# Optimization experiments

Hardware: AMD Instinct MI355X
Metric: run time of the kernel (lower is better)

Reference implementation:

```python
import jax, jax.numpy as jnp
import numpy as np


def _temperature():
    # Reproduce the per-class temperature from RIDE.__init__
    cls_num_list = np.array([705, 717, 281, 4772, 1982, 1290, 2524], dtype=np.float64)
    p = cls_num_list / cls_num_list.sum()
    C = len(cls_num_list)
    w = C * p * 0.015 + 1 - 0.015
    w = w / w.max()
    return jnp.asarray(1.5 * w, dtype=jnp.float32)[None, :]  # (1, C)


def setup_inputs() -> dict:
    key = jax.random.key(0)
    k1, k2, k3, k4, k5 = jax.random.split(key, 5)
    N, C = 2097152, 7
    return {
        "outputs1": jax.random.normal(k1, (N, C), dtype=jnp.float32),
        "outputs2": jax.random.normal(k2, (N, C), dtype=jnp.float32),
        "outputs3": jax.random.normal(k3, (N, C), dtype=jnp.float32),
        "outputs4": jax.random.normal(k4, (N, C), dtype=jnp.float32),
        "targets": jax.random.randint(k5, (N,), 0, C, dtype=jnp.int64),
    }


def reference(outputs1, outputs2, outputs3, outputs4, targets):
    # targets is unused by the original loss math (only logits enter the KL terms).
    T = _temperature()                       # (1, C), broadcasts over batch
    mT2 = jnp.mean(T * T)                    # scalar: mean over classes of T^2

    z0 = outputs1 / T                        # (N, C)
    q = jax.nn.softmax(z0, axis=-1)          # teacher probs
    logq = jax.nn.log_softmax(z0, axis=-1)

    def kl_mean(out_j):
        # KLDivLoss(reduction='mean') over a single-sample (1, C) slice == mean over C
        lp = jax.nn.log_softmax(out_j / T, axis=-1)
        return jnp.mean(q * (logq - lp), axis=-1)  # (N,)

    cost = kl_mean(outputs2) + kl_mean(outputs3) + kl_mean(outputs4)  # (N,)
    # KD_loss (scalar) * T * T then .mean(1) == KD_loss * mean(T^2); d = cost/3
    loss = cost * mT2 / 3.0
    return jnp.mean(loss)
```

## Files before the change

kernel.cpp:

```cpp
#include <hip/hip_runtime.h>


struct RideConsts {
    float invT[7];
    float scale;
};


#define STUDENT_ROW(R, c0, c1, c2, c3, c4, c5, c6) do {                      \
    const float z0 = (c0) * iT0, z1 = (c1) * iT1, z2 = (c2) * iT2,           \
                z3 = (c3) * iT3, z4 = (c4) * iT4, z5 = (c5) * iT5,           \
                z6 = (c6) * iT6;                                             \
    const float m = fmaxf(fmaxf(fmaxf(z0, z1), fmaxf(z2, z3)),              \
                          fmaxf(fmaxf(z4, z5), z6));                         \
    const float S = __expf(z0 - m) + __expf(z1 - m) + __expf(z2 - m) +       \
                    __expf(z3 - m) + __expf(z4 - m) + __expf(z5 - m) +       \
                    __expf(z6 - m);                                          \
    zs##R##0 += z0; zs##R##1 += z1; zs##R##2 += z2; zs##R##3 += z3;          \
    zs##R##4 += z4; zs##R##5 += z5; zs##R##6 += z6;                          \
    mls##R += m + __logf(S);                                                 \
} while (0)

#define TEACHER_ROW(R, c0, c1, c2, c3, c4, c5, c6) do {                      \
    const float z0 = (c0) * iT0, z1 = (c1) * iT1, z2 = (c2) * iT2,           \
                z3 = (c3) * iT3, z4 = (c4) * iT4, z5 = (c5) * iT5,           \
                z6 = (c6) * iT6;                                             \
    const float m = fmaxf(fmaxf(fmaxf(z0, z1), fmaxf(z2, z3)),              \
                          fmaxf(fmaxf(z4, z5), z6));                         \
    const float e0 = __expf(z0 - m), e1 = __expf(z1 - m),                    \
                e2 = __expf(z2 - m), e3 = __expf(z3 - m),                    \
                e4 = __expf(z4 - m), e5 = __expf(z5 - m),                    \
                e6 = __expf(z6 - m);                                         \
    const float S = e0 + e1 + e2 + e3 + e4 + e5 + e6;                        \
    const float invS = 1.0f / S, mlogS = m + __logf(S);                      \
    const float q0 = e0 * invS, q1 = e1 * invS, q2 = e2 * invS,              \
                q3 = e3 * invS, q4 = e4 * invS, q5 = e5 * invS,              \
                q6 = e6 * invS;                                              \
    const float qz = q0 * z0 + q1 * z1 + q2 * z2 + q3 * z3 + q4 * z4 +       \
                     q5 * z5 + q6 * z6;                                      \
    const float dot = q0 * zs##R##0 + q1 * zs##R##1 + q2 * zs##R##2 +        \
                      q3 * zs##R##3 + q4 * zs##R##4 + q5 * zs##R##5 +        \
                      q6 * zs##R##6;                                         \
    cost += 3.0f * (qz - mlogS) - dot + mls##R;                              \
} while (0)

#define DO_ARRAY(ROWM, ptr) do {                                             \
    const float4* gp = (const float4*)(ptr) + base;                          \
    const float4 g0 = gp[0], g1 = gp[1], g2 = gp[2], g3 = gp[3],             \
                 g4 = gp[4], g5 = gp[5], g6 = gp[6];                         \
    ROWM(0, g0.x, g0.y, g0.z, g0.w, g1.x, g1.y, g1.z);                       \
    ROWM(1, g1.w, g2.x, g2.y, g2.z, g2.w, g3.x, g3.y);                       \
    ROWM(2, g3.z, g3.w, g4.x, g4.y, g4.z, g4.w, g5.x);                       \
    ROWM(3, g5.y, g5.z, g5.w, g6.x, g6.y, g6.z, g6.w);                       \
} while (0)

__global__ __launch_bounds__(256, 5) void ride_main(
    const float* __restrict__ x1, const float* __restrict__ x2,
    const float* __restrict__ x3, const float* __restrict__ x4,
    float* __restrict__ partials, RideConsts cst)
{
    const int t = threadIdx.x;
    const int w = t >> 6;
    const int L = t & 63;
    const int waveId = blockIdx.x * 4 + w;

    const size_t base = (size_t)waveId * 448 + (size_t)L * 7;

    const float iT0 = cst.invT[0], iT1 = cst.invT[1], iT2 = cst.invT[2],
                iT3 = cst.invT[3], iT4 = cst.invT[4], iT5 = cst.invT[5],
                iT6 = cst.invT[6];

    float zs00 = 0, zs01 = 0, zs02 = 0, zs03 = 0, zs04 = 0, zs05 = 0, zs06 = 0;
    float zs10 = 0, zs11 = 0, zs12 = 0, zs13 = 0, zs14 = 0, zs15 = 0, zs16 = 0;
    float zs20 = 0, zs21 = 0, zs22 = 0, zs23 = 0, zs24 = 0, zs25 = 0, zs26 = 0;
    float zs30 = 0, zs31 = 0, zs32 = 0, zs33 = 0, zs34 = 0, zs35 = 0, zs36 = 0;
    float mls0 = 0, mls1 = 0, mls2 = 0, mls3 = 0;

    DO_ARRAY(STUDENT_ROW, x2);
    DO_ARRAY(STUDENT_ROW, x3);
    DO_ARRAY(STUDENT_ROW, x4);

    float cost = 0.0f;
    DO_ARRAY(TEACHER_ROW, x1);

    cost *= cst.scale;

#pragma unroll
    for (int off = 32; off > 0; off >>= 1)
        cost += __shfl_down(cost, off, 64);
    if (L == 0) partials[waveId] = cost;
}

__global__ __launch_bounds__(256) void ride_reduce(
    const float* __restrict__ p, float* __restrict__ out, int n4)
{
    const float4* p4 = (const float4*)p;
    float s = 0.0f;
    for (int i = threadIdx.x; i < n4; i += 256) {
        float4 v = p4[i];
        s += (v.x + v.y) + (v.z + v.w);
    }
#pragma unroll
    for (int off = 32; off > 0; off >>= 1)
        s += __shfl_down(s, off, 64);
    __shared__ float red[4];
    if ((threadIdx.x & 63) == 0) red[threadIdx.x >> 6] = s;
    __syncthreads();
    if (threadIdx.x == 0) out[0] = red[0] + red[1] + red[2] + red[3];
}

extern "C" void kernel_launch(void* const* d_in, const int* in_sizes, int n_in,
                              void* d_out, int out_size, void* d_ws, size_t ws_size,
                              hipStream_t stream)
{
    const float* x1 = (const float*)d_in[0];
    const float* x2 = (const float*)d_in[1];
    const float* x3 = (const float*)d_in[2];
    const float* x4 = (const float*)d_in[3];

    const int N = in_sizes[0] / 7;

    RideConsts cst;
    {
        const double cls[7] = {705, 717, 281, 4772, 1982, 1290, 2524};
        double sum = 0.0;
        for (int c = 0; c < 7; ++c) sum += cls[c];
        double w[7], wmax = 0.0;
        for (int c = 0; c < 7; ++c) {
            const double p = cls[c] / sum;
            w[c] = 7.0 * p * 0.015 + 1.0 - 0.015;
            if (w[c] > wmax) wmax = w[c];
        }
        double mT2 = 0.0;
        for (int c = 0; c < 7; ++c) {
            const float T = (float)(1.5 * (w[c] / wmax));
            cst.invT[c] = 1.0f / T;
            mT2 += (double)T * (double)T;
        }
        mT2 /= 7.0;
        cst.scale = (float)(mT2 / (3.0 * (double)N * 7.0));
    }

    const int nWaves = N / 256;
    const int grid   = nWaves / 4;

    float* partials = (float*)d_ws;

    ride_main<<<grid, 256, 0, stream>>>(x1, x2, x3, x4, partials, cst);
    ride_reduce<<<1, 256, 0, stream>>>(partials, (float*)d_out, nWaves / 4);
}
```

Baseline: 230.2 us.

## Stream rows through double-buffered LDS with global_load_lds in persistent waves

Replaces direct per-thread float4 loads with a loop in which each wave processes four chunks of 256 rows. Each chunk is fetched from global memory into LDS with the async global_load_lds builtin, double-buffered so the next array's load overlaps compute on the current one. The grid is fixed at 2048 waves and occupancy hints are lowered to allow the larger LDS footprint. This aims at better memory-level parallelism and coalesced loads, at the cost of LDS reads with a stride-7 bank pattern, manual waitcnt correctness, and a hardcoded wave count that only covers N = 2097152.

```diff
diff --git a/kernel.cpp b/kernel.cpp
--- a/kernel.cpp
+++ b/kernel.cpp
@@ -1,4 +1,5 @@
 #include <hip/hip_runtime.h>
+#include <stdint.h>
 
 
 struct RideConsts {
@@ -6,12 +7,34 @@
     float scale;
 };
 
+#define AS1 __attribute__((address_space(1)))
+#define AS3 __attribute__((address_space(3)))
+
+#define GLL16(g, l)                                                          \
+    __builtin_amdgcn_global_load_lds((AS1 void*)(void*)(g),                  \
+                                     (AS3 void*)(void*)(l), 16, 0, 0)
+
+#define WAITVM(n)  asm volatile("s_waitcnt vmcnt(" #n ")" ::: "memory")
+#define WAITLGKM() asm volatile("s_waitcnt lgkmcnt(0)" ::: "memory")
+
+#define PREFETCH(arr, c, bufIdx) do {                                        \
+    const float4* gp_ = (const float4*)(arr) + wbase + (size_t)(c) * 448 + L;\
+    float* lp_ = myLds + (bufIdx) * 1792;                                    \
+    GLL16(gp_ + 0 * 64, lp_ + 0 * 256);                                      \
+    GLL16(gp_ + 1 * 64, lp_ + 1 * 256);                                      \
+    GLL16(gp_ + 2 * 64, lp_ + 2 * 256);                                      \
+    GLL16(gp_ + 3 * 64, lp_ + 3 * 256);                                      \
+    GLL16(gp_ + 4 * 64, lp_ + 4 * 256);                                      \
+    GLL16(gp_ + 5 * 64, lp_ + 5 * 256);                                      \
+    GLL16(gp_ + 6 * 64, lp_ + 6 * 256);                                      \
+} while (0)
+
 
 #define STUDENT_ROW(R, c0, c1, c2, c3, c4, c5, c6) do {                      \
     const float z0 = (c0) * iT0, z1 = (c1) * iT1, z2 = (c2) * iT2,           \
                 z3 = (c3) * iT3, z4 = (c4) * iT4, z5 = (c5) * iT5,           \
                 z6 = (c6) * iT6;                                             \
-    const float m = fmaxf(fmaxf(fmaxf(z0, z1), fmaxf(z2, z3)),              \
+    const float m = fmaxf(fmaxf(fmaxf(z0, z1), fmaxf(z2, z3)),               \
                           fmaxf(fmaxf(z4, z5), z6));                         \
     const float S = __expf(z0 - m) + __expf(z1 - m) + __expf(z2 - m) +       \
                     __expf(z3 - m) + __expf(z4 - m) + __expf(z5 - m) +       \
@@ -25,7 +48,7 @@
     const float z0 = (c0) * iT0, z1 = (c1) * iT1, z2 = (c2) * iT2,           \
                 z3 = (c3) * iT3, z4 = (c4) * iT4, z5 = (c5) * iT5,           \
                 z6 = (c6) * iT6;                                             \
-    const float m = fmaxf(fmaxf(fmaxf(z0, z1), fmaxf(z2, z3)),              \
+    const float m = fmaxf(fmaxf(fmaxf(z0, z1), fmaxf(z2, z3)),               \
                           fmaxf(fmaxf(z4, z5), z6));                         \
     const float e0 = __expf(z0 - m), e1 = __expf(z1 - m),                    \
                 e2 = __expf(z2 - m), e3 = __expf(z3 - m),                    \
@@ -44,27 +67,52 @@
     cost += 3.0f * (qz - mlogS) - dot + mls##R;                              \
 } while (0)
 
-#define DO_ARRAY(ROWM, ptr) do {                                             \
-    const float4* gp = (const float4*)(ptr) + base;                          \
-    const float4 g0 = gp[0], g1 = gp[1], g2 = gp[2], g3 = gp[3],             \
-                 g4 = gp[4], g5 = gp[5], g6 = gp[6];                         \
-    ROWM(0, g0.x, g0.y, g0.z, g0.w, g1.x, g1.y, g1.z);                       \
-    ROWM(1, g1.w, g2.x, g2.y, g2.z, g2.w, g3.x, g3.y);                       \
-    ROWM(2, g3.z, g3.w, g4.x, g4.y, g4.z, g4.w, g5.x);                       \
-    ROWM(3, g5.y, g5.z, g5.w, g6.x, g6.y, g6.z, g6.w);                       \
-} while (0)
-
-__global__ __launch_bounds__(256, 5) void ride_main(
+#define STUDENT_STEP(bufIdx) do {                                            \
+    const float* b_ = myLds + (bufIdx) * 1792 + 7 * L;                       \
+    STUDENT_ROW(0, b_[0],    b_[1],    b_[2],    b_[3],                      \
+                   b_[4],    b_[5],    b_[6]);                               \
+    STUDENT_ROW(1, b_[448],  b_[449],  b_[450],  b_[451],                    \
+                   b_[452],  b_[453],  b_[454]);                             \
+    STUDENT_ROW(2, b_[896],  b_[897],  b_[898],  b_[899],                    \
+                   b_[900],  b_[901],  b_[902]);                             \
+    STUDENT_ROW(3, b_[1344], b_[1345], b_[1346], b_[1347],                   \
+                   b_[1348], b_[1349], b_[1350]);                            \
+} while (0)
+
+#define TEACHER_STEP(bufIdx) do {                                            \
+    const float* b_ = myLds + (bufIdx) * 1792 + 7 * L;                       \
+    TEACHER_ROW(0, b_[0],    b_[1],    b_[2],    b_[3],                      \
+                   b_[4],    b_[5],    b_[6]);                               \
+    TEACHER_ROW(1, b_[448],  b_[449],  b_[450],  b_[451],                    \
+                   b_[452],  b_[453],  b_[454]);                             \
+    TEACHER_ROW(2, b_[896],  b_[897],  b_[898],  b_[899],                    \
+                   b_[900],  b_[901],  b_[902]);                             \
+    TEACHER_ROW(3, b_[1344], b_[1345], b_[1346], b_[1347],                   \
+                   b_[1348], b_[1349], b_[1350]);                            \
+} while (0)
+
+#define RESET_CHUNK() do {                                                   \
+    zs00 = 0; zs01 = 0; zs02 = 0; zs03 = 0; zs04 = 0; zs05 = 0; zs06 = 0;    \
+    zs10 = 0; zs11 = 0; zs12 = 0; zs13 = 0; zs14 = 0; zs15 = 0; zs16 = 0;    \
+    zs20 = 0; zs21 = 0; zs22 = 0; zs23 = 0; zs24 = 0; zs25 = 0; zs26 = 0;    \
+    zs30 = 0; zs31 = 0; zs32 = 0; zs33 = 0; zs34 = 0; zs35 = 0; zs36 = 0;    \
+    mls0 = 0; mls1 = 0; mls2 = 0; mls3 = 0;                                  \
+} while (0)
+
+__global__ __launch_bounds__(256, 2) void ride_main(
     const float* __restrict__ x1, const float* __restrict__ x2,
     const float* __restrict__ x3, const float* __restrict__ x4,
     float* __restrict__ partials, RideConsts cst)
 {
+    __shared__ __align__(16) float lds[4][2 * 1792];
+
     const int t = threadIdx.x;
     const int w = t >> 6;
     const int L = t & 63;
     const int waveId = blockIdx.x * 4 + w;
-
-    const size_t base = (size_t)waveId * 448 + (size_t)L * 7;
+    float* myLds = &lds[w][0];
+
+    const size_t wbase = (size_t)waveId * 1792;
 
     const float iT0 = cst.invT[0], iT1 = cst.invT[1], iT2 = cst.invT[2],
                 iT3 = cst.invT[3], iT4 = cst.invT[4], iT5 = cst.invT[5],
@@ -75,13 +123,32 @@
     float zs20 = 0, zs21 = 0, zs22 = 0, zs23 = 0, zs24 = 0, zs25 = 0, zs26 = 0;
     float zs30 = 0, zs31 = 0, zs32 = 0, zs33 = 0, zs34 = 0, zs35 = 0, zs36 = 0;
     float mls0 = 0, mls1 = 0, mls2 = 0, mls3 = 0;
-
-    DO_ARRAY(STUDENT_ROW, x2);
-    DO_ARRAY(STUDENT_ROW, x3);
-    DO_ARRAY(STUDENT_ROW, x4);
-
     float cost = 0.0f;
-    DO_ARRAY(TEACHER_ROW, x1);
+
+    PREFETCH(x2, 0, 0);
+
+#pragma unroll
+    for (int s = 0; s < 16; ++s) {
+        const int a = s & 3;
+        if (s + 1 < 16) {
+            const int ns = s + 1;
+            const int na = ns & 3, nc = ns >> 2;
+            const float* narr = (na == 0) ? x2 : (na == 1) ? x3
+                              : (na == 2) ? x4 : x1;
+            WAITLGKM();
+            PREFETCH(narr, nc, ns & 1);
+            WAITVM(7);
+        } else {
+            WAITVM(0);
+        }
+
+        if (a < 3) {
+            STUDENT_STEP(s & 1);
+        } else {
+            TEACHER_STEP(s & 1);
+            RESET_CHUNK();
+        }
+    }
 
     cost *= cst.scale;
 
@@ -141,7 +208,7 @@
         cst.scale = (float)(mT2 / (3.0 * (double)N * 7.0));
     }
 
-    const int nWaves = N / 256;
+    const int nWaves = 2048;
     const int grid   = nWaves / 4;
 
     float* partials = (float*)d_ws;
```

Result: no change. 229.8 us (-0.1%).
